# Optimization experiments

Measured on AMD Instinct MI355X. Metric: run time of the kernel, lower is better.

Reference implementation:

```python
import jax, jax.numpy as jnp
import numpy as np


def _relative_position_index(S):
    # Faithful to the torch buffer construction, computed once with numpy (static).
    coords = np.stack(np.meshgrid(np.arange(S), np.arange(S), indexing='ij'))  # (2,S,S)
    coords = coords.reshape(2, -1)                                             # (2,N)
    rel = coords[:, :, None] - coords[:, None, :]                              # (2,N,N)
    rel = rel.transpose(1, 2, 0).astype(np.int64)                              # (N,N,2)
    rel[:, :, 0] += S - 1
    rel[:, :, 1] += S - 1
    rel[:, :, 0] *= 2 * S - 1
    idx = rel.sum(-1)
    idx = idx[::-1, ::-1].copy()  # flipud(fliplr(...))
    return idx                    # (N,N) int64 in [0, (2S-1)^2)


def setup_inputs() -> dict:
    key = jax.random.key(0)
    ks = jax.random.split(key, 6)
    B, S, C, NH = 8, 32, 512, 16
    x = jax.random.normal(ks[0], (B, S, S, C), dtype=jnp.float32)
    qkv_w = jax.random.normal(ks[1], (3 * C, C), dtype=jnp.float32) * 0.02
    qkv_b = jax.random.normal(ks[2], (3 * C,), dtype=jnp.float32) * 0.02
    rpb = jax.random.normal(ks[3], (NH, 2 * S - 1, 2 * S - 1), dtype=jnp.float32) * 0.02
    proj_w = jax.random.normal(ks[4], (C, C), dtype=jnp.float32) * 0.02
    proj_b = jax.random.normal(ks[5], (C,), dtype=jnp.float32) * 0.02
    return {"x": x, "qkv_w": qkv_w, "qkv_b": qkv_b, "rpb": rpb,
            "proj_w": proj_w, "proj_b": proj_b}


def reference(x, qkv_w, qkv_b, rpb, proj_w, proj_b):
    B, H, W, C = x.shape
    N = H * W
    num_heads = rpb.shape[0]
    head_dim = C // num_heads
    scale = head_dim ** (-0.5)
    S = H

    idx = _relative_position_index(S)  # static numpy (N,N)

    qkv = x.reshape(B, N, C) @ qkv_w.T + qkv_b            # (B,N,3C)
    qkv = qkv.reshape(B, N, 3, num_heads, head_dim)
    qkv = jnp.transpose(qkv, (2, 0, 3, 1, 4))             # (3,B,h,N,d)
    q, k, v = qkv[0], qkv[1], qkv[2]

    attn = jnp.einsum('bhnd,bhmd->bhnm', q * scale, k)    # (B,h,N,N)
    # gather relative position bias: (h,(2S-1)^2)[:, idx] -> (h,N,N)
    bias = rpb.reshape(num_heads, -1)[:, idx]
    attn = jax.nn.softmax(attn + bias[None], axis=-1)

    out = jnp.einsum('bhnm,bhmd->bhnd', attn, v)          # (B,h,N,d)
    out = jnp.transpose(out, (0, 2, 1, 3)).reshape(B, H, W, C)
    return out @ proj_w.T + proj_b
```

## Files before the change

### kernel.cpp

```cpp
#include <hip/hip_runtime.h>

typedef __bf16 bf16x8 __attribute__((ext_vector_type(8)));
typedef float f32x4 __attribute__((ext_vector_type(4)));
typedef unsigned int u32x2 __attribute__((ext_vector_type(2)));
typedef unsigned short u16;
typedef unsigned int u32;

__device__ __forceinline__ float bf2f(u16 v) {
    union { unsigned u; float f; } x; x.u = ((unsigned)v) << 16; return x.f;
}
__device__ __forceinline__ u16 f2bf(float f) {
    union { float f; unsigned u; } x; x.f = f;
    unsigned r = x.u + 0x7fffu + ((x.u >> 16) & 1u);
    return (u16)(r >> 16);
}

__device__ __forceinline__ bool probe_is_f32(const void* xp) {
    const unsigned* p = (const unsigned*)xp;
    int hits = 0;
#pragma unroll
    for (int i = 0; i < 32; i++) {
        const unsigned e = (p[i] >> 7) & 0xffu;
        hits += (e >= 0x90u) ? 1 : 0;
    }
    return hits > 3;
}

__device__ __forceinline__ float ld1(const void* p, size_t i, bool isf32) {
    return isf32 ? ((const float*)p)[i] : bf2f(((const u16*)p)[i]);
}

__device__ __forceinline__ void gl2lds16(const void* g, void* l) {
    __builtin_amdgcn_global_load_lds(
        (const __attribute__((address_space(1))) u32*)g,
        (__attribute__((address_space(3))) u32*)l, 16, 0, 0);
}

__global__ __launch_bounds__(256)
void convert_inputs(const void* __restrict__ x, const void* __restrict__ qw,
                    const void* __restrict__ qb, const void* __restrict__ pw,
                    const void* __restrict__ pb, const void* __restrict__ rp,
                    u16* __restrict__ xbf, u16* __restrict__ qwbf,
                    u16* __restrict__ qbbf, u16* __restrict__ pwbf,
                    u16* __restrict__ pbbf, float* __restrict__ rpl2e)
{
    const bool isf32 = probe_is_f32(x);
    const int gid = blockIdx.x * 256 + threadIdx.x;
    const int gsz = gridDim.x * 256;

    struct Seg { const void* s; u16* d; int n; };
    const Seg segs[5] = {{x, xbf, 4194304}, {qw, qwbf, 786432}, {pw, pwbf, 262144},
                         {qb, qbbf, 1536}, {pb, pbbf, 512}};
    for (int t = 0; t < 5; t++) {
        const int n4 = segs[t].n >> 2;
        if (isf32) {
            const f32x4* s = (const f32x4*)segs[t].s;
            for (int i = gid; i < n4; i += gsz) {
                f32x4 v = s[i];
                ushort4 o;
                o.x = f2bf(v[0]); o.y = f2bf(v[1]); o.z = f2bf(v[2]); o.w = f2bf(v[3]);
                *(ushort4*)(segs[t].d + i * 4) = o;
            }
        } else {
            const ushort4* s = (const ushort4*)segs[t].s;
            for (int i = gid; i < n4; i += gsz) *(ushort4*)(segs[t].d + i * 4) = s[i];
        }
    }
    for (int i = gid; i < 63504; i += gsz)
        rpl2e[i] = ld1(rp, i, isf32) * 1.4426950408889634f;
}

template<int MODE, int BM>
__global__ __launch_bounds__(256, MODE == 1 ? 3 : 4)
void gemm_bt(const u16* __restrict__ A, const u16* __restrict__ W,
             const u16* __restrict__ bias, void* __restrict__ out,
             u16* __restrict__ q_out, u16* __restrict__ k_out, u16* __restrict__ v_out,
             const void* __restrict__ probe, int Nout, int K)
{
    __shared__ __align__(16) u16 As[2][BM * 32];
    __shared__ __align__(16) u16 Ws[2][128 * 32];
    constexpr int RW = BM / 32;

    const int tid  = threadIdx.x;
    const int lane = tid & 63;
    const int wave = tid >> 6;
    const int quad = lane >> 4;
    const int l16  = lane & 15;
    const int m0 = blockIdx.y * BM;
    const int n0 = blockIdx.x * 128;
    const int wm = (wave >> 1) * (BM / 2);
    const int wn = (wave & 1) * 64;

    f32x4 acc[RW][4] = {};

    for (int k0 = 0; k0 < K; k0 += 64) {
        __syncthreads();
        for (int u = 0; u < 2; u++) {
            {
                const u16* g = A + (size_t)(m0 + wave * 16 + (lane >> 2)) * K
                                 + k0 + u * 32 + (lane & 3) * 8;
                u16* l = As[u] + wave * 16 * 32;
                for (int p = 0; p < BM / 64; p++) gl2lds16(g + (size_t)p * 64 * K, l + p * 64 * 32);
            }
            {
                const u16* g = W + (size_t)(n0 + wave * 16 + (lane >> 2)) * K
                                 + k0 + u * 32 + (lane & 3) * 8;
                u16* l = Ws[u] + wave * 16 * 32;
                for (int p = 0; p < 2; p++) gl2lds16(g + (size_t)p * 64 * K, l + p * 64 * 32);
            }
        }
        __syncthreads();

        for (int u = 0; u < 2; u++) {
            bf16x8 af[RW], wf[4];
            for (int i = 0; i < RW; i++)
                af[i] = *(const bf16x8*)(As[u] + (wm + i * 16 + l16) * 32 + quad * 8);
            for (int j = 0; j < 4; j++)
                wf[j] = *(const bf16x8*)(Ws[u] + (wn + j * 16 + l16) * 32 + quad * 8);
            for (int i = 0; i < RW; i++)
                for (int j = 0; j < 4; j++)
                    acc[i][j] = __builtin_amdgcn_mfma_f32_16x16x32_bf16(af[i], wf[j], acc[i][j], 0, 0, 0);
        }
    }

    if (MODE == 0) {
        const bool isf32 = probe_is_f32(probe);
        for (int j = 0; j < 4; j++) {
            const int col = n0 + wn + j * 16 + l16;
            const float bv = bf2f(bias[col]);
            for (int i = 0; i < RW; i++) {
                const int rbase = m0 + wm + i * 16 + quad * 4;
                for (int r = 0; r < 4; r++) {
                    const float val = acc[i][j][r] + bv;
                    if (isf32) ((float*)out)[(size_t)(rbase + r) * Nout + col] = val;
                    else       ((u16*)out)[(size_t)(rbase + r) * Nout + col]  = f2bf(val);
                }
            }
        }
    } else {
        const int which = m0 >> 9;
        u16* dst = which == 0 ? q_out : (which == 1 ? k_out : v_out);
        const float qsc = (which == 0) ? 0.25503485724582146f : 1.0f;
        float bv[RW][4];
        for (int i = 0; i < RW; i++) {
            const int row4 = m0 + wm + i * 16 + quad * 4;
            for (int r = 0; r < 4; r++) bv[i][r] = bf2f(bias[row4 + r]) * qsc;
        }
        for (int j = 0; j < 4; j++) {
            const int tok = n0 + wn + j * 16 + l16;
            const int bi = tok >> 10, t = tok & 1023;
            for (int i = 0; i < RW; i++) {
                ushort4 pk;
                pk.x = f2bf(acc[i][j][0] * qsc + bv[i][0]);
                pk.y = f2bf(acc[i][j][1] * qsc + bv[i][1]);
                pk.z = f2bf(acc[i][j][2] * qsc + bv[i][2]);
                pk.w = f2bf(acc[i][j][3] * qsc + bv[i][3]);
                const int row4 = m0 + wm + i * 16 + quad * 4;
                const int h = (row4 >> 5) & 15;
                const int c = row4 & 31;
                *(ushort4*)(dst + ((size_t)(bi * 16 + h) * 1024 + t) * 32 + c) = pk;
            }
        }
    }
}

__global__ __launch_bounds__(256, 4)
void attn(const u16* __restrict__ q, const u16* __restrict__ k,
          const u16* __restrict__ v, const float* __restrict__ rpl2e,
          u16* __restrict__ o)
{
    __shared__ __align__(16) u16 Ks[2][64 * 40];
    __shared__ __align__(16) u16 Vt[2][32 * 72];
    __shared__ float biasT[63 * 37];

    const int tid  = threadIdx.x;
    const int lane = tid & 63;
    const int wave = tid >> 6;
    const int quad = lane >> 4;
    const int l16  = lane & 15;

    const int h  = blockIdx.x;
    const int qt = blockIdx.y;
    const int b  = blockIdx.z;
    const int n0 = qt * 128;
    const size_t base = ((size_t)(b * 16 + h)) * 32768;

    {
        const int row0 = 28 - 4 * qt;
        for (int idx = tid; idx < 2205; idx += 256) {
            const int rr = idx / 63, cc = idx % 63;
            biasT[cc * 37 + rr] =
                rpl2e[(size_t)h * 3969 + (size_t)(row0 + rr) * 63 + cc];
        }
    }
    const int vt_t = lane;
    const int vcg  = wave;
    uint4 kreg = *(const uint4*)(k + base + (size_t)(tid >> 2) * 32 + (tid & 3) * 8);
    uint4 vreg = *(const uint4*)(v + base + (size_t)vt_t * 32 + vcg * 8);
    *(uint4*)(Ks[0] + (tid >> 2) * 40 + (tid & 3) * 8) = kreg;
    {
        const u16* vr = (const u16*)&vreg;
#pragma unroll
        for (int jj = 0; jj < 8; jj++)
            Vt[0][(vcg * 8 + jj) * 72 + vt_t] = vr[jj];
    }

    bf16x8 qf[2];
    for (int g = 0; g < 2; g++) {
        union { uint4 u; bf16x8 f; } cv;
        cv.u = *(const uint4*)(q + base + (size_t)(n0 + g * 64 + wave * 16 + l16) * 32 + quad * 8);
        qf[g] = cv.f;
    }
    __syncthreads();

    bf16x8 ones;
    for (int i = 0; i < 8; i++) ones[i] = (__bf16)1.0f;

    f32x4 o_acc[2][3] = {};
    const int bn = (wave & 1) * 16 + l16;
    const int w2 = wave >> 1;

    const int cb = quad * 4 + 31 - bn;
    f32x4 X0v[2], X1v[2], Y0v[2], Y1v[2];
#pragma unroll
    for (int p2 = 0; p2 < 2; p2++)
#pragma unroll
        for (int r = 0; r < 4; r++) {
            const int c37 = (cb + p2 * 16 + r) * 37;
            X0v[p2][r] = biasT[c37 + (1 - w2)];
            X1v[p2][r] = biasT[c37 + (2 - w2)];
            Y0v[p2][r] = biasT[c37 + (3 - w2)];
            Y1v[p2][r] = biasT[c37 + (4 - w2)];
        }

    for (int kt = 0; kt < 16; kt++) {
        const int cur = kt & 1;
        if (kt < 15) {
            const int mn = (kt + 1) * 64;
            kreg = *(const uint4*)(k + base + (size_t)(mn + (tid >> 2)) * 32 + (tid & 3) * 8);
            vreg = *(const uint4*)(v + base + (size_t)(mn + vt_t) * 32 + vcg * 8);
        }

        bf16x8 kf[4];
#pragma unroll
        for (int j = 0; j < 4; j++)
            kf[j] = *(const bf16x8*)(Ks[cur] + (j * 16 + l16) * 40 + quad * 8);
        bf16x8 vf[2][2];
#pragma unroll
        for (int kc = 0; kc < 2; kc++)
#pragma unroll
            for (int ct = 0; ct < 2; ct++)
                vf[kc][ct] = *(const bf16x8*)(Vt[cur] + (ct * 16 + l16) * 72 + kc * 32 + quad * 8);

#pragma unroll
        for (int g = 0; g < 2; g++) {
            f32x4 s4[4];
#pragma unroll
            for (int j = 0; j < 4; j++) {
                const f32x4 Cb = g ? ((j >> 1) ? X1v[j & 1] : X0v[j & 1])
                                   : ((j >> 1) ? Y1v[j & 1] : Y0v[j & 1]);
                s4[j] = __builtin_amdgcn_mfma_f32_16x16x32_bf16(kf[j], qf[g], Cb, 0, 0, 0);
            }

            u32 Aw[4], Bw[4];
#pragma unroll
            for (int j = 0; j < 4; j++) {
                u16 pk[4];
#pragma unroll
                for (int r = 0; r < 4; r++) {
                    const float pv = __builtin_amdgcn_exp2f(s4[j][r]);
                    union { __bf16 b; u16 u; } cv; cv.b = (__bf16)pv;
                    pk[r] = cv.u;
                }
                Aw[j] = ((u32)pk[1] << 16) | pk[0];
                Bw[j] = ((u32)pk[3] << 16) | pk[2];
            }

#pragma unroll
            for (int kc = 0; kc < 2; kc++) {
                u32x2 ra = __builtin_amdgcn_permlane32_swap(Aw[2 * kc], Aw[2 * kc + 1], false, false);
                u32x2 wa = __builtin_amdgcn_permlane16_swap(ra.x, ra.y, false, false);
                u32x2 rb = __builtin_amdgcn_permlane32_swap(Bw[2 * kc], Bw[2 * kc + 1], false, false);
                u32x2 wb = __builtin_amdgcn_permlane16_swap(rb.x, rb.y, false, false);
                union { u32 w[4]; bf16x8 f; } pa;
                pa.w[0] = wa.x; pa.w[1] = wb.x; pa.w[2] = wa.y; pa.w[3] = wb.y;
#pragma unroll
                for (int ct = 0; ct < 2; ct++)
                    o_acc[g][ct] = __builtin_amdgcn_mfma_f32_16x16x32_bf16(pa.f, vf[kc][ct], o_acc[g][ct], 0, 0, 0);
                o_acc[g][2] = __builtin_amdgcn_mfma_f32_16x16x32_bf16(pa.f, ones, o_acc[g][2], 0, 0, 0);
            }
        }

        if (kt < 15) {
#pragma unroll
            for (int p2 = 0; p2 < 2; p2++) { X0v[p2] = Y0v[p2]; X1v[p2] = Y1v[p2]; }
            const int nr = 2 * kt - w2 + 5;
#pragma unroll
            for (int p2 = 0; p2 < 2; p2++)
#pragma unroll
                for (int r = 0; r < 4; r++) {
                    const int c37 = (cb + p2 * 16 + r) * 37;
                    Y0v[p2][r] = biasT[c37 + nr];
                    Y1v[p2][r] = biasT[c37 + nr + 1];
                }
            *(uint4*)(Ks[cur ^ 1] + (tid >> 2) * 40 + (tid & 3) * 8) = kreg;
            const u16* vr = (const u16*)&vreg;
#pragma unroll
            for (int jj = 0; jj < 8; jj++)
                Vt[cur ^ 1][(vcg * 8 + jj) * 72 + vt_t] = vr[jj];
        }
        __syncthreads();
    }

    for (int g = 0; g < 2; g++)
        for (int r = 0; r < 4; r++) {
            const float inv = __builtin_amdgcn_rcpf(o_acc[g][2][r]);
            const int n = n0 + g * 64 + wave * 16 + quad * 4 + r;
            u16* orow = o + ((size_t)b * 1024 + n) * 512 + h * 32;
            orow[l16]      = f2bf(o_acc[g][0][r] * inv);
            orow[16 + l16] = f2bf(o_acc[g][1][r] * inv);
        }
}

extern "C" void kernel_launch(void* const* d_in, const int* in_sizes, int n_in,
                              void* d_out, int out_size, void* d_ws, size_t ws_size,
                              hipStream_t stream) {
    const void* x      = d_in[0];
    const void* qkv_w  = d_in[1];
    const void* qkv_b  = d_in[2];
    const void* rpb    = d_in[3];
    const void* proj_w = d_in[4];
    const void* proj_b = d_in[5];

    u16* ws    = (u16*)d_ws;
    u16* kb    = ws;
    u16* vb    = ws + 4194304;
    u16* xbf   = ws + 8388608;
    u16* ao    = xbf;
    u16* qwbf  = ws + 12582912;
    u16* pwbf  = ws + 13369344;
    u16* qbbf  = ws + 13631488;
    u16* pbbf  = ws + 13633024;
    float* rpl2e = (float*)(ws + 13633536);
    u16* qb    = (u16*)d_out;

    convert_inputs<<<1024, 256, 0, stream>>>(x, qkv_w, qkv_b, proj_w, proj_b, rpb,
                                             xbf, qwbf, qbbf, pwbf, pbbf, rpl2e);

    dim3 g1(8192 / 128, 1536 / 128);
    gemm_bt<1, 128><<<g1, 256, 0, stream>>>(qwbf, xbf, qbbf, nullptr, qb, kb, vb, x, 8192, 512);

    dim3 g2(16, 8, 8);
    attn<<<g2, 256, 0, stream>>>(qb, kb, vb, rpl2e, ao);

    dim3 g3(512 / 128, 8192 / 64);
    gemm_bt<0, 64><<<g3, 256, 0, stream>>>(ao, pwbf, pbbf, d_out, nullptr, nullptr, nullptr, x, 512, 512);
}
```

Before: 146.8 us.

## Software-pipeline GEMM K loop with double-buffered async LDS prefetch

Restructures the bf16 MFMA GEMM main loop to step in 32-wide K slices. The next slice's global-to-LDS copies are issued into the alternate buffer before the current slice's MFMAs run. Global and LDS base pointers are hoisted, the inner loops are fully unrolled, and one barrier per step replaces two, so memory latency can overlap compute. The risk is that correctness now depends on the async LDS loads for the current slice having completed by the single barrier.

Measured after the change: 150.4 us. 2.4% more time.

```diff
diff --git a/kernel.cpp b/kernel.cpp
--- a/kernel.cpp
+++ b/kernel.cpp
@@ -91,36 +91,45 @@
     const int wm = (wave >> 1) * (BM / 2);
     const int wn = (wave & 1) * 64;
 
+    const u16* gA0 = A + (size_t)(m0 + wave * 16 + (lane >> 2)) * K + (lane & 3) * 8;
+    const u16* gW0 = W + (size_t)(n0 + wave * 16 + (lane >> 2)) * K + (lane & 3) * 8;
+    u16* lA = As[0] + wave * 16 * 32;
+    u16* lW = Ws[0] + wave * 16 * 32;
+    constexpr int ABUF = BM * 32;
+    constexpr int WBUF = 128 * 32;
+
+    auto issue = [&](int s) {
+        const int buf = s & 1;
+        const u16* ga = gA0 + s * 32;
+        const u16* gw = gW0 + s * 32;
+#pragma unroll
+        for (int p = 0; p < BM / 64; p++)
+            gl2lds16(ga + (size_t)p * 64 * K, lA + buf * ABUF + p * 64 * 32);
+#pragma unroll
+        for (int p = 0; p < 2; p++)
+            gl2lds16(gw + (size_t)p * 64 * K, lW + buf * WBUF + p * 64 * 32);
+    };
+
     f32x4 acc[RW][4] = {};
 
-    for (int k0 = 0; k0 < K; k0 += 64) {
+    const int NS = K >> 5;
+    issue(0);
+    for (int s = 0; s < NS; s++) {
         __syncthreads();
-        for (int u = 0; u < 2; u++) {
-            {
-                const u16* g = A + (size_t)(m0 + wave * 16 + (lane >> 2)) * K
-                                 + k0 + u * 32 + (lane & 3) * 8;
-                u16* l = As[u] + wave * 16 * 32;
-                for (int p = 0; p < BM / 64; p++) gl2lds16(g + (size_t)p * 64 * K, l + p * 64 * 32);
-            }
-            {
-                const u16* g = W + (size_t)(n0 + wave * 16 + (lane >> 2)) * K
-                                 + k0 + u * 32 + (lane & 3) * 8;
-                u16* l = Ws[u] + wave * 16 * 32;
-                for (int p = 0; p < 2; p++) gl2lds16(g + (size_t)p * 64 * K, l + p * 64 * 32);
-            }
-        }
-        __syncthreads();
-
-        for (int u = 0; u < 2; u++) {
-            bf16x8 af[RW], wf[4];
-            for (int i = 0; i < RW; i++)
-                af[i] = *(const bf16x8*)(As[u] + (wm + i * 16 + l16) * 32 + quad * 8);
+        if (s < NS - 1) issue(s + 1);
+        const int buf = s & 1;
+        bf16x8 af[RW], wf[4];
+#pragma unroll
+        for (int i = 0; i < RW; i++)
+            af[i] = *(const bf16x8*)(As[buf] + (wm + i * 16 + l16) * 32 + quad * 8);
+#pragma unroll
+        for (int j = 0; j < 4; j++)
+            wf[j] = *(const bf16x8*)(Ws[buf] + (wn + j * 16 + l16) * 32 + quad * 8);
+#pragma unroll
+        for (int i = 0; i < RW; i++)
+#pragma unroll
             for (int j = 0; j < 4; j++)
-                wf[j] = *(const bf16x8*)(Ws[u] + (wn + j * 16 + l16) * 32 + quad * 8);
-            for (int i = 0; i < RW; i++)
-                for (int j = 0; j < 4; j++)
-                    acc[i][j] = __builtin_amdgcn_mfma_f32_16x16x32_bf16(af[i], wf[j], acc[i][j], 0, 0, 0);
-        }
+                acc[i][j] = __builtin_amdgcn_mfma_f32_16x16x32_bf16(af[i], wf[j], acc[i][j], 0, 0, 0);
     }
 
     if (MODE == 0) {
```
